# Performance work log

Hardware: AMD Instinct MI355X
Metric: run time of the kernel (lower is better)

## Reference

```python
import jax, jax.numpy as jnp
import numpy as np

B, S, H, NH = 2, 2048, 1024, 16
HD = H // NH  # 64


def setup_inputs() -> dict:
    key = jax.random.key(0)
    ks = jax.random.split(key, 11)
    sc = 1.0 / np.sqrt(H)
    inp = {
        "q": jax.random.normal(ks[0], (B, S, H), dtype=jnp.float32),
        "k": jax.random.normal(ks[1], (B, S, H), dtype=jnp.float32),
        "v": jax.random.normal(ks[2], (B, S, H), dtype=jnp.float32),
        # nn.Linear params: weight [out,in], bias [out]
        "wq_w": jax.random.normal(ks[3], (H, H), dtype=jnp.float32) * sc,
        "wq_b": jnp.zeros((H,), dtype=jnp.float32),
        "wk_w": jax.random.normal(ks[4], (H, H), dtype=jnp.float32) * sc,
        "wk_b": jnp.zeros((H,), dtype=jnp.float32),
        "wv_w": jax.random.normal(ks[5], (H, H), dtype=jnp.float32) * sc,
        "wv_b": jnp.zeros((H,), dtype=jnp.float32),
        "wo_w": jax.random.normal(ks[6], (H, H), dtype=jnp.float32) * sc,
        "wo_b": jnp.zeros((H,), dtype=jnp.float32),
    }
    return inp


def _split_heads(x):
    # [B,S,H] -> [B,NH,S,HD]
    b, s, _ = x.shape
    return x.reshape(b, s, NH, HD).transpose(0, 2, 1, 3)


def reference(q, k, v, wq_w, wq_b, wk_w, wk_b, wv_w, wv_b, wo_w, wo_b):
    qw = q @ wq_w.T + wq_b
    kw = k @ wk_w.T + wk_b
    vw = v @ wv_w.T + wv_b
    hq = _split_heads(qw)  # [B,NH,S,HD]
    hk = _split_heads(kw)
    hv = _split_heads(vw)
    scale = 1.0 / jnp.sqrt(jnp.float32(HD))
    scores = jnp.einsum("bhqd,bhkd->bhqk", hq, hk) * scale  # [B,NH,S,S]
    attn = jax.nn.softmax(scores, axis=-1)
    out = jnp.einsum("bhqk,bhkd->bhqd", attn, hv)  # [B,NH,S,HD]
    out = out.transpose(0, 2, 1, 3).reshape(q.shape[0], -1, H)  # [B,S,H]
    final = out @ wo_w.T + wo_b
    return final, attn
```

## Files before the change

kernel.cpp:

```cpp
#include <hip/hip_runtime.h>

typedef short bf16x8 __attribute__((ext_vector_type(8)));
typedef float f32x4 __attribute__((ext_vector_type(4)));
typedef unsigned short ushort4v __attribute__((ext_vector_type(4)));
typedef unsigned short ushort8 __attribute__((ext_vector_type(8)));

#define DEVI static __device__ __forceinline__

DEVI unsigned short f2bf(float f) {
    unsigned u = __float_as_uint(f);
    u += 0x7FFFu + ((u >> 16) & 1u);
    return (unsigned short)(u >> 16);
}

DEVI unsigned cvtpk(float lo, float hi) {
    unsigned r;
    asm("v_cvt_pk_bf16_f32 %0, %1, %2" : "=v"(r) : "v"(lo), "v"(hi));
    return r;
}

typedef __attribute__((address_space(3))) unsigned int* lds_ptr_t;
typedef const __attribute__((address_space(1))) unsigned int* gbl_ptr_t;
#define GLDS(gp, lp) __builtin_amdgcn_global_load_lds((gbl_ptr_t)(gp), (lds_ptr_t)(lp), 16, 0, 0)

__global__ void cvt_kernel(const float* __restrict__ src, unsigned short* __restrict__ dst, int n) {
    int i = (blockIdx.x * 256 + threadIdx.x) * 4;
    if (i >= n) return;
    float4 v = *(const float4*)(src + i);
    ushort4v o;
    o.x = f2bf(v.x); o.y = f2bf(v.y); o.z = f2bf(v.z); o.w = f2bf(v.w);
    *(ushort4v*)(dst + i) = o;
}

__global__ void cvt2_kernel(const float* __restrict__ s0, unsigned short* __restrict__ d0, int n0,
                            const float* __restrict__ s1, unsigned short* __restrict__ d1, int n1) {
    int idx = blockIdx.x * 256 + threadIdx.x;
    const int c0 = n0 >> 2;
    const float* src; unsigned short* dst; int i;
    if (idx < c0) { src = s0; dst = d0; i = idx * 4; }
    else {
        i = (idx - c0) * 4;
        if (i >= n1) return;
        src = s1; dst = d1;
    }
    float4 v = *(const float4*)(src + i);
    ushort4v o;
    o.x = f2bf(v.x); o.y = f2bf(v.y); o.z = f2bf(v.z); o.w = f2bf(v.w);
    *(ushort4v*)(dst + i) = o;
}

__global__ void cvt4_kernel(const float* __restrict__ q, const float* __restrict__ k,
                            const float* __restrict__ v, const float* __restrict__ wq,
                            const float* __restrict__ wk, const float* __restrict__ wv,
                            const float* __restrict__ wo, unsigned short* __restrict__ dq,
                            unsigned short* __restrict__ dk, unsigned short* __restrict__ dv,
                            unsigned short* __restrict__ dwq, unsigned short* __restrict__ dwk,
                            unsigned short* __restrict__ dwv, unsigned short* __restrict__ dwo) {
    int idx = blockIdx.x * 256 + threadIdx.x;
    const float* src; unsigned short* dst; int base;
    if (idx < 1048576) { src = q; dst = dq; base = idx; }
    else if (idx < 2097152) { src = k; dst = dk; base = idx - 1048576; }
    else if (idx < 3145728) { src = v; dst = dv; base = idx - 2097152; }
    else if (idx < 3407872) { src = wq; dst = dwq; base = idx - 3145728; }
    else if (idx < 3670016) { src = wk; dst = dwk; base = idx - 3407872; }
    else if (idx < 3932160) { src = wv; dst = dwv; base = idx - 3670016; }
    else { src = wo; dst = dwo; base = idx - 3932160; }
    const int i = base * 4;
    float4 x = *(const float4*)(src + i);
    ushort4v o;
    o.x = f2bf(x.x); o.y = f2bf(x.y); o.z = f2bf(x.z); o.w = f2bf(x.w);
    *(ushort4v*)(dst + i) = o;
}

#define GEMM_BODY(A, W)                                                                             \
    constexpr int K = 1024;                                                                         \
    __shared__ unsigned short Asb[2][64 * 32];                                                      \
    __shared__ unsigned short Bsb[2][128 * 32];                                                     \
    const int t = threadIdx.x;                                                                      \
    const int w = t >> 6, l = t & 63;                                                               \
    const int wr = w >> 1, wc = w & 1;                                                              \
    const int fr = l & 15, fg = l >> 4;                                                             \
    const int m0 = blockIdx.y * 64, n0 = blockIdx.x * 128;                                          \
    const int ra = t >> 2, qa = (t & 3) * 8;                                                        \
    const int c1 = 256 + t, rb1 = c1 >> 2, qb1 = (c1 & 3) * 8;                                      \
    f32x4 acc[2][4] = {};                                                                           \
    GLDS(A + (size_t)(m0 + ra) * K + qa, &Asb[0][t * 8]);                                           \
    GLDS(W + (size_t)(n0 + ra) * K + qa, &Bsb[0][t * 8]);                                           \
    GLDS(W + (size_t)(n0 + rb1) * K + qb1, &Bsb[0][c1 * 8]);                                        \
    for (int t2 = 0; t2 < 32; ++t2) {                                                               \
        const int cur = t2 & 1;                                                                     \
        if (t2 < 31) {                                                                              \
            const int kb = (t2 + 1) * 32;                                                           \
            GLDS(A + (size_t)(m0 + ra) * K + kb + qa, &Asb[cur ^ 1][t * 8]);                        \
            GLDS(W + (size_t)(n0 + ra) * K + kb + qa, &Bsb[cur ^ 1][t * 8]);                        \
            GLDS(W + (size_t)(n0 + rb1) * K + kb + qb1, &Bsb[cur ^ 1][c1 * 8]);                     \
            asm volatile("s_waitcnt vmcnt(3)" ::: "memory");                                        \
        } else {                                                                                    \
            asm volatile("s_waitcnt vmcnt(0)" ::: "memory");                                        \
        }                                                                                           \
        __syncthreads();                                                                            \
        bf16x8 af[2], bfv[4];                                                                       \
        _Pragma("unroll") for (int mi = 0; mi < 2; mi++)                                            \
            af[mi] = *(const bf16x8*)(&Asb[cur][(wr * 32 + mi * 16 + fr) * 32 + fg * 8]);           \
        _Pragma("unroll") for (int ni = 0; ni < 4; ni++)                                            \
            bfv[ni] = *(const bf16x8*)(&Bsb[cur][(wc * 64 + ni * 16 + fr) * 32 + fg * 8]);          \
        _Pragma("unroll") for (int mi = 0; mi < 2; mi++)                                            \
            _Pragma("unroll") for (int ni = 0; ni < 4; ni++)                                        \
                acc[mi][ni] = __builtin_amdgcn_mfma_f32_16x16x32_bf16(af[mi], bfv[ni], acc[mi][ni], 0, 0, 0); \
        __syncthreads();                                                                            \
    }

template <int MODE>
__global__ __launch_bounds__(256) void gemm_bt(const unsigned short* __restrict__ A,
                                               const unsigned short* __restrict__ W,
                                               const float* __restrict__ bias,
                                               void* __restrict__ Cout) {
    GEMM_BODY(A, W)
#pragma unroll
    for (int ni = 0; ni < 4; ni++) {
        const int n = n0 + wc * 64 + ni * 16 + fr;
        const float bv = bias[n];
#pragma unroll
        for (int mi = 0; mi < 2; mi++) {
            const int mb = m0 + wr * 32 + mi * 16 + fg * 4;
            if constexpr (MODE == 1) {
                float* C = (float*)Cout;
#pragma unroll
                for (int r = 0; r < 4; r++) C[(size_t)(mb + r) * 1024 + n] = acc[mi][ni][r] + bv;
            } else if constexpr (MODE == 0) {
                unsigned short* C = (unsigned short*)Cout;
                const int h = n >> 6, hd = n & 63;
#pragma unroll
                for (int r = 0; r < 4; r++) {
                    const int m = mb + r;
                    const int bb = m >> 11, s = m & 2047;
                    C[(size_t)((bb * 16 + h) * 2048 + s) * 64 + hd] = f2bf(acc[mi][ni][r] + bv);
                }
            } else {
                unsigned short* C = (unsigned short*)Cout;
                const int h = n >> 6, hd = n & 63;
                const int bb = mb >> 11, s = mb & 2047;
                const int blk = s >> 6, off = s & 63;
                const int pos = blk * 64 + (off >> 5) * 32 + ((off & 15) >> 2) * 8 + ((off >> 4) & 1) * 4;
                ushort4v pk;
                pk.x = f2bf(acc[mi][ni][0] + bv);
                pk.y = f2bf(acc[mi][ni][1] + bv);
                pk.z = f2bf(acc[mi][ni][2] + bv);
                pk.w = f2bf(acc[mi][ni][3] + bv);
                *(ushort4v*)(C + (size_t)((bb * 16 + h) * 64 + hd) * 2048 + pos) = pk;
            }
        }
    }
}

__global__ __launch_bounds__(256) void gemm_qkv(const unsigned short* __restrict__ Aq,
                                                const unsigned short* __restrict__ Ak,
                                                const unsigned short* __restrict__ Av,
                                                const unsigned short* __restrict__ Wq,
                                                const unsigned short* __restrict__ Wk,
                                                const unsigned short* __restrict__ Wv,
                                                const float* __restrict__ bq,
                                                const float* __restrict__ bk,
                                                const float* __restrict__ bv_,
                                                unsigned short* __restrict__ qh,
                                                unsigned short* __restrict__ kh,
                                                unsigned short* __restrict__ vt) {
    const int z = blockIdx.z;
    const unsigned short* A = (z == 0) ? Aq : (z == 1) ? Ak : Av;
    const unsigned short* W = (z == 0) ? Wq : (z == 1) ? Wk : Wv;
    const float* bias = (z == 0) ? bq : (z == 1) ? bk : bv_;
    GEMM_BODY(A, W)
#pragma unroll
    for (int ni = 0; ni < 4; ni++) {
        const int n = n0 + wc * 64 + ni * 16 + fr;
        const float bv = bias[n];
        const int h = n >> 6, hd = n & 63;
#pragma unroll
        for (int mi = 0; mi < 2; mi++) {
            const int mb = m0 + wr * 32 + mi * 16 + fg * 4;
            if (z == 2) {
                const int bb = mb >> 11, s = mb & 2047;
                const int blk = s >> 6, off = s & 63;
                const int pos = blk * 64 + (off >> 5) * 32 + ((off & 15) >> 2) * 8 + ((off >> 4) & 1) * 4;
                ushort4v pk;
                pk.x = f2bf(acc[mi][ni][0] + bv);
                pk.y = f2bf(acc[mi][ni][1] + bv);
                pk.z = f2bf(acc[mi][ni][2] + bv);
                pk.w = f2bf(acc[mi][ni][3] + bv);
                *(ushort4v*)(vt + (size_t)((bb * 16 + h) * 64 + hd) * 2048 + pos) = pk;
            } else {
                unsigned short* C = (z == 0) ? qh : kh;
#pragma unroll
                for (int r = 0; r < 4; r++) {
                    const int m = mb + r;
                    const int bb = m >> 11, s = m & 2047;
                    C[(size_t)((bb * 16 + h) * 2048 + s) * 64 + hd] = f2bf(acc[mi][ni][r] + bv);
                }
            }
        }
    }
}

__global__ __launch_bounds__(256, 2) void attn_kernel(const unsigned short* __restrict__ Qh,
                                                      const unsigned short* __restrict__ Kh,
                                                      const unsigned short* __restrict__ Vt,
                                                      unsigned short* __restrict__ Obuf,
                                                      float* __restrict__ AttnOut) {
    __shared__ float rpart[32][4];
    __shared__ float rinv_s[32];
    __shared__ float ored[32][68];

    const int i = blockIdx.x;
    const int qt = i & 63, bh = i >> 6;
    const int b = bh >> 4, h = bh & 15;
    const int q0 = qt * 32;
    const int t = threadIdx.x, w = t >> 6, l = t & 63;
    const int fr = l & 15, fg = l >> 4;
    const float SCL = 0.1803368801111f;

    const unsigned short* qb = Qh + (size_t)(bh * 2048 + q0) * 64;
    bf16x8 qf[2][2];
#pragma unroll
    for (int qs = 0; qs < 2; qs++)
#pragma unroll
        for (int kc = 0; kc < 2; kc++)
            qf[qs][kc] = *(const bf16x8*)(qb + (size_t)(qs * 16 + fr) * 64 + kc * 32 + fg * 8);

    const unsigned short* kbase = Kh + ((size_t)bh * 2048 + w * 512) * 64;
    const unsigned short* vtb = Vt + (size_t)bh * 64 * 2048;

    unsigned p0[8][8], p1[8][8];
    float rs0 = 0.f, rs1 = 0.f;
#pragma unroll
    for (int kt = 0; kt < 8; ++kt) {
#pragma unroll
        for (int mt = 0; mt < 4; ++mt) {
            const unsigned short* kr = kbase + (size_t)(kt * 64 + mt * 16 + fr) * 64 + fg * 8;
            bf16x8 kf0 = *(const bf16x8*)kr;
            bf16x8 kf1 = *(const bf16x8*)(kr + 32);
            f32x4 d0 = {}, d1 = {};
            d0 = __builtin_amdgcn_mfma_f32_16x16x32_bf16(kf0, qf[0][0], d0, 0, 0, 0);
            d0 = __builtin_amdgcn_mfma_f32_16x16x32_bf16(kf1, qf[0][1], d0, 0, 0, 0);
            d1 = __builtin_amdgcn_mfma_f32_16x16x32_bf16(kf0, qf[1][0], d1, 0, 0, 0);
            d1 = __builtin_amdgcn_mfma_f32_16x16x32_bf16(kf1, qf[1][1], d1, 0, 0, 0);
            const float a0 = exp2f(d0[0] * SCL), a1 = exp2f(d0[1] * SCL);
            const float a2 = exp2f(d0[2] * SCL), a3 = exp2f(d0[3] * SCL);
            rs0 += (a0 + a1) + (a2 + a3);
            p0[kt][mt * 2] = cvtpk(a0, a1);
            p0[kt][mt * 2 + 1] = cvtpk(a2, a3);
            const float c0 = exp2f(d1[0] * SCL), c1 = exp2f(d1[1] * SCL);
            const float c2 = exp2f(d1[2] * SCL), c3 = exp2f(d1[3] * SCL);
            rs1 += (c0 + c1) + (c2 + c3);
            p1[kt][mt * 2] = cvtpk(c0, c1);
            p1[kt][mt * 2 + 1] = cvtpk(c2, c3);
        }
    }
    rs0 += __shfl_xor(rs0, 16, 64); rs0 += __shfl_xor(rs0, 32, 64);
    rs1 += __shfl_xor(rs1, 16, 64); rs1 += __shfl_xor(rs1, 32, 64);
    if (l < 16) { rpart[l][w] = rs0; rpart[l + 16][w] = rs1; }
    __syncthreads();
    for (int j = t; j < 32 * 68; j += 256) (&ored[0][0])[j] = 0.f;
    if (t < 32) rinv_s[t] = 1.0f / (rpart[t][0] + rpart[t][1] + rpart[t][2] + rpart[t][3]);
    __syncthreads();
    const float ri0 = rinv_s[fr], ri1 = rinv_s[16 + fr];

    float* attnB0 = AttnOut + (size_t)bh * 2048 * 2048 + (size_t)(q0 + fr) * 2048 + w * 512;
    float* attnB1 = attnB0 + (size_t)16 * 2048;
    f32x4 opv[2][4] = {};
#pragma unroll
    for (int kt = 0; kt < 8; ++kt) {
        bf16x8 vf[2][4];
#pragma unroll
        for (int kc = 0; kc < 2; ++kc)
#pragma unroll
            for (int dt = 0; dt < 4; ++dt)
                vf[kc][dt] = *(const bf16x8*)(vtb + (size_t)(dt * 16 + fr) * 2048 + w * 512 + kt * 64 + kc * 32 + fg * 8);
#pragma unroll
        for (int mt = 0; mt < 4; ++mt) {
            const unsigned a = p0[kt][mt * 2], aa = p0[kt][mt * 2 + 1];
            f32x4 o;
            o[0] = __uint_as_float(a << 16) * ri0;
            o[1] = __uint_as_float(a & 0xffff0000u) * ri0;
            o[2] = __uint_as_float(aa << 16) * ri0;
            o[3] = __uint_as_float(aa & 0xffff0000u) * ri0;
            __builtin_nontemporal_store(o, (f32x4*)(attnB0 + kt * 64 + mt * 16 + fg * 4));
            const unsigned c = p1[kt][mt * 2], cc = p1[kt][mt * 2 + 1];
            f32x4 o1;
            o1[0] = __uint_as_float(c << 16) * ri1;
            o1[1] = __uint_as_float(c & 0xffff0000u) * ri1;
            o1[2] = __uint_as_float(cc << 16) * ri1;
            o1[3] = __uint_as_float(cc & 0xffff0000u) * ri1;
            __builtin_nontemporal_store(o1, (f32x4*)(attnB1 + kt * 64 + mt * 16 + fg * 4));
        }
#pragma unroll
        for (int kc = 0; kc < 2; ++kc) {
            union { unsigned u[4]; bf16x8 v; } pb0, pb1;
#pragma unroll
            for (int j = 0; j < 4; j++) { pb0.u[j] = p0[kt][4 * kc + j]; pb1.u[j] = p1[kt][4 * kc + j]; }
#pragma unroll
            for (int dt = 0; dt < 4; ++dt) {
                opv[0][dt] = __builtin_amdgcn_mfma_f32_16x16x32_bf16(vf[kc][dt], pb0.v, opv[0][dt], 0, 0, 0);
                opv[1][dt] = __builtin_amdgcn_mfma_f32_16x16x32_bf16(vf[kc][dt], pb1.v, opv[1][dt], 0, 0, 0);
            }
        }
    }

    __syncthreads();
    for (int ww = 0; ww < 4; ++ww) {
        if (w == ww) {
#pragma unroll
            for (int qs = 0; qs < 2; qs++)
#pragma unroll
                for (int dt = 0; dt < 4; dt++)
#pragma unroll
                    for (int r = 0; r < 4; r++)
                        ored[qs * 16 + fr][dt * 16 + 4 * fg + r] += opv[qs][dt][r];
        }
        __syncthreads();
    }
    {
        const int row = t >> 3, cb = (t & 7) * 8;
        const float rr = rinv_s[row];
        ushort8 pk;
#pragma unroll
        for (int j = 0; j < 8; j++) pk[j] = f2bf(ored[row][cb + j] * rr);
        *(ushort8*)(Obuf + (size_t)(b * 2048 + q0 + row) * 1024 + h * 64 + cb) = pk;
    }
}

extern "C" void kernel_launch(void* const* d_in, const int* in_sizes, int n_in,
                              void* d_out, int out_size, void* d_ws, size_t ws_size,
                              hipStream_t stream) {
    const float* q = (const float*)d_in[0];
    const float* k = (const float*)d_in[1];
    const float* v = (const float*)d_in[2];
    const float* wqw = (const float*)d_in[3];
    const float* wqb = (const float*)d_in[4];
    const float* wkw = (const float*)d_in[5];
    const float* wkb = (const float*)d_in[6];
    const float* wvw = (const float*)d_in[7];
    const float* wvb = (const float*)d_in[8];
    const float* wow = (const float*)d_in[9];
    const float* wob = (const float*)d_in[10];

    float* finalOut = (float*)d_out;
    float* attnOut = finalOut + 4194304;
    char* ws = (char*)d_ws;

    const int NX = 4194304, NW = 1048576;
    dim3 gGrid(8, 64);

    if (ws_size >= 67108864ull) {
        unsigned short* qbf  = (unsigned short*)(ws);
        unsigned short* kbf  = (unsigned short*)(ws + 8388608);
        unsigned short* vbf  = (unsigned short*)(ws + 16777216);
        unsigned short* wqbf = (unsigned short*)(ws + 25165824);
        unsigned short* wkbf = (unsigned short*)(ws + 27262976);
        unsigned short* wvbf = (unsigned short*)(ws + 29360128);
        unsigned short* wobf = (unsigned short*)(ws + 31457280);
        unsigned short* qh   = (unsigned short*)(ws + 33554432);
        unsigned short* kh   = (unsigned short*)(ws + 41943040);
        unsigned short* vt   = (unsigned short*)(ws + 50331648);
        unsigned short* obuf = (unsigned short*)(ws + 58720256);

        cvt4_kernel<<<16384, 256, 0, stream>>>(q, k, v, wqw, wkw, wvw, wow,
                                               qbf, kbf, vbf, wqbf, wkbf, wvbf, wobf);
        dim3 g3(8, 64, 3);
        gemm_qkv<<<g3, 256, 0, stream>>>(qbf, kbf, vbf, wqbf, wkbf, wvbf,
                                         wqb, wkb, wvb, qh, kh, vt);
        attn_kernel<<<2048, 256, 0, stream>>>(qh, kh, vt, obuf, attnOut);
        gemm_bt<1><<<gGrid, 256, 0, stream>>>(obuf, wobf, wob, finalOut);
    } else {
        unsigned short* xbf  = (unsigned short*)(ws);
        unsigned short* wbf  = (unsigned short*)(ws + 8388608);
        unsigned short* qh   = (unsigned short*)(ws + 10485760);
        unsigned short* kh   = (unsigned short*)(ws + 18874368);
        unsigned short* vt   = (unsigned short*)(ws + 27262976);
        unsigned short* obuf = (unsigned short*)(ws + 35651584);
        const int c2grid = (NX + NW) / 1024;

        cvt2_kernel<<<c2grid, 256, 0, stream>>>(q, xbf, NX, wqw, wbf, NW);
        gemm_bt<0><<<gGrid, 256, 0, stream>>>(xbf, wbf, wqb, qh);
        cvt2_kernel<<<c2grid, 256, 0, stream>>>(k, xbf, NX, wkw, wbf, NW);
        gemm_bt<0><<<gGrid, 256, 0, stream>>>(xbf, wbf, wkb, kh);
        cvt2_kernel<<<c2grid, 256, 0, stream>>>(v, xbf, NX, wvw, wbf, NW);
        gemm_bt<2><<<gGrid, 256, 0, stream>>>(xbf, wbf, wvb, vt);
        attn_kernel<<<2048, 256, 0, stream>>>(qh, kh, vt, obuf, attnOut);
        cvt_kernel<<<NW / 1024, 256, 0, stream>>>(wow, wbf, NW);
        gemm_bt<1><<<gGrid, 256, 0, stream>>>(obuf, wbf, wob, finalOut);
    }
}
```

Measured before the change: 283.5 us.

## Enlarge QKV GEMM tile to 128x128 with double-buffered LDS staging

The fused QKV projection GEMM gets its own 128x128 tile main loop in place of the shared GEMM_BODY. It double-buffers async global-to-LDS loads with explicit vmcnt waits and halves the grid along M, so each warp computes a 64x64 block with 16 MFMA accumulators. Separately, the attention kernel no longer zero-fills the output reduction buffer; the first warp's pass writes to it directly. The larger tile improves data reuse and overlaps loads with compute, at the cost of more registers and fewer blocks.

Measured after the change: 269.8 us. -4.8%, faster.

```diff
diff --git a/kernel.cpp b/kernel.cpp
--- a/kernel.cpp
+++ b/kernel.cpp
@@ -165,19 +165,68 @@
                                                 unsigned short* __restrict__ qh,
                                                 unsigned short* __restrict__ kh,
                                                 unsigned short* __restrict__ vt) {
+    constexpr int K = 1024;
+    __shared__ unsigned short Asb[2][128 * 32];
+    __shared__ unsigned short Bsb[2][128 * 32];
     const int z = blockIdx.z;
     const unsigned short* A = (z == 0) ? Aq : (z == 1) ? Ak : Av;
     const unsigned short* W = (z == 0) ? Wq : (z == 1) ? Wk : Wv;
     const float* bias = (z == 0) ? bq : (z == 1) ? bk : bv_;
-    GEMM_BODY(A, W)
+
+    const int t = threadIdx.x;
+    const int w = t >> 6, l = t & 63;
+    const int wr = w >> 1, wc = w & 1;
+    const int fr = l & 15, fg = l >> 4;
+    const int m0 = blockIdx.y * 128, n0 = blockIdx.x * 128;
+
+    const int c0 = t, c1 = 256 + t;
+    const int r0 = c0 >> 2, q0off = (c0 & 3) * 8;
+    const int r1 = c1 >> 2, q1off = (c1 & 3) * 8;
+
+    f32x4 acc[4][4] = {};
+
+#define STG128(kb, pb)                                                        \
+    {                                                                         \
+        GLDS(A + (size_t)(m0 + r0) * K + (kb) + q0off, &Asb[pb][c0 * 8]);     \
+        GLDS(A + (size_t)(m0 + r1) * K + (kb) + q1off, &Asb[pb][c1 * 8]);     \
+        GLDS(W + (size_t)(n0 + r0) * K + (kb) + q0off, &Bsb[pb][c0 * 8]);     \
+        GLDS(W + (size_t)(n0 + r1) * K + (kb) + q1off, &Bsb[pb][c1 * 8]);     \
+    }
+
+    STG128(0, 0);
+    for (int t2 = 0; t2 < 32; ++t2) {
+        const int cur = t2 & 1;
+        if (t2 < 31) {
+            STG128((t2 + 1) * 32, cur ^ 1);
+            asm volatile("s_waitcnt vmcnt(4)" ::: "memory");
+        } else {
+            asm volatile("s_waitcnt vmcnt(0)" ::: "memory");
+        }
+        __syncthreads();
+        bf16x8 af[4], bfv[4];
+#pragma unroll
+        for (int mi = 0; mi < 4; mi++)
+            af[mi] = *(const bf16x8*)(&Asb[cur][(wr * 64 + mi * 16 + fr) * 32 + fg * 8]);
+#pragma unroll
+        for (int ni = 0; ni < 4; ni++)
+            bfv[ni] = *(const bf16x8*)(&Bsb[cur][(wc * 64 + ni * 16 + fr) * 32 + fg * 8]);
+#pragma unroll
+        for (int mi = 0; mi < 4; mi++)
+#pragma unroll
+            for (int ni = 0; ni < 4; ni++)
+                acc[mi][ni] = __builtin_amdgcn_mfma_f32_16x16x32_bf16(af[mi], bfv[ni], acc[mi][ni], 0, 0, 0);
+        __syncthreads();
+    }
+#undef STG128
+
 #pragma unroll
     for (int ni = 0; ni < 4; ni++) {
         const int n = n0 + wc * 64 + ni * 16 + fr;
         const float bv = bias[n];
         const int h = n >> 6, hd = n & 63;
 #pragma unroll
-        for (int mi = 0; mi < 2; mi++) {
-            const int mb = m0 + wr * 32 + mi * 16 + fg * 4;
+        for (int mi = 0; mi < 4; mi++) {
+            const int mb = m0 + wr * 64 + mi * 16 + fg * 4;
             if (z == 2) {
                 const int bb = mb >> 11, s = mb & 2047;
                 const int blk = s >> 6, off = s & 63;
@@ -259,7 +308,6 @@
     rs1 += __shfl_xor(rs1, 16, 64); rs1 += __shfl_xor(rs1, 32, 64);
     if (l < 16) { rpart[l][w] = rs0; rpart[l + 16][w] = rs1; }
     __syncthreads();
-    for (int j = t; j < 32 * 68; j += 256) (&ored[0][0])[j] = 0.f;
     if (t < 32) rinv_s[t] = 1.0f / (rpart[t][0] + rpart[t][1] + rpart[t][2] + rpart[t][3]);
     __syncthreads();
     const float ri0 = rinv_s[fr], ri1 = rinv_s[16 + fr];
@@ -313,8 +361,12 @@
 #pragma unroll
                 for (int dt = 0; dt < 4; dt++)
 #pragma unroll
-                    for (int r = 0; r < 4; r++)
-                        ored[qs * 16 + fr][dt * 16 + 4 * fg + r] += opv[qs][dt][r];
+                    for (int r = 0; r < 4; r++) {
+                        if (ww == 0)
+                            ored[qs * 16 + fr][dt * 16 + 4 * fg + r] = opv[qs][dt][r];
+                        else
+                            ored[qs * 16 + fr][dt * 16 + 4 * fg + r] += opv[qs][dt][r];
+                    }
         }
         __syncthreads();
     }
@@ -365,7 +417,7 @@
 
         cvt4_kernel<<<16384, 256, 0, stream>>>(q, k, v, wqw, wkw, wvw, wow,
                                                qbf, kbf, vbf, wqbf, wkbf, wvbf, wobf);
-        dim3 g3(8, 64, 3);
+        dim3 g3(8, 32, 3);
         gemm_qkv<<<g3, 256, 0, stream>>>(qbf, kbf, vbf, wqbf, wkbf, wvbf,
                                          wqb, wkb, wvb, qh, kh, vt);
         attn_kernel<<<2048, 256, 0, stream>>>(qh, kh, vt, obuf, attnOut);
```
